# Performance work log

Measured on AMD Instinct MI355X. Metric: run time of the kernel, lower is better.

## Reference

```python
import jax, jax.numpy as jnp
import numpy as np


def setup_inputs() -> dict:
    key = jax.random.key(0)
    kW, kH, kT = jax.random.split(key, 3)
    N, M, rank = 1024, 1024, 64
    W = jax.random.uniform(kW, (N, rank), dtype=jnp.float32)
    H = jax.random.uniform(kH, (rank, M), dtype=jnp.float32)
    tau = jax.random.uniform(kT, (N, rank), dtype=jnp.float32)
    return {"W": W, "H": H, "tau": tau}


def reference(W, H, tau):
    # Vectorized ShiftNMF forward over all M frequency bins at once.
    # Original: for f in range(M): WHt[:, f] = (softplus(W) * exp(-1j*2*pi*f/M * tau)) @ Hf[:, f]
    M = H.shape[1]
    Hf = jnp.fft.fft(jax.nn.softplus(H), axis=1)          # (rank, M) complex64
    Wp = jax.nn.softplus(W)                                # (N, rank)
    freqs = jnp.arange(M, dtype=jnp.float32)               # (M,)
    # phase[n, r, f] = exp(-1j * 2*pi*f/M * tau[n, r])
    phase = jnp.exp((-2j * jnp.pi / M) * tau[:, :, None] * freqs[None, None, :])  # (N, rank, M)
    # WHt[n, f] = sum_r Wp[n, r] * phase[n, r, f] * Hf[r, f]
    WHt = jnp.einsum('nr,nrf,rf->nf', Wp.astype(phase.dtype), phase, Hf)
    return WHt
```

## Files before the change

kernel.cpp:

```cpp
#include <hip/hip_runtime.h>
#include <math.h>

#define M_DIM 1024
#define N_DIM 1024
#define NRANK 64
#define BN 16
#define BF 64

typedef float f32x2 __attribute__((ext_vector_type(2)));

__device__ f32x2 g_Hf[NRANK * M_DIM];

__device__ __forceinline__ float softplus_f(float x) {
    return log1pf(__expf(x));
}

__device__ __forceinline__ float fast_sin_rev(float rev) {
#if __has_builtin(__builtin_amdgcn_sinf)
    return __builtin_amdgcn_sinf(rev);
#else
    return __sinf(rev * 6.28318530717958647f);
#endif
}
__device__ __forceinline__ float fast_cos_rev(float rev) {
#if __has_builtin(__builtin_amdgcn_cosf)
    return __builtin_amdgcn_cosf(rev);
#else
    return __cosf(rev * 6.28318530717958647f);
#endif
}

__global__ __launch_bounds__(512) void fft_rows(const float* __restrict__ H) {
    __shared__ float sre[M_DIM];
    __shared__ float sim[M_DIM];
    const int r = blockIdx.x;
    const int tid = threadIdx.x;

    for (int j = tid; j < M_DIM; j += 512) {
        int src = __brev((unsigned)j) >> 22;
        sre[j] = softplus_f(H[r * M_DIM + src]);
        sim[j] = 0.0f;
    }
    __syncthreads();

    int log2half = 0;
    for (int len = 2; len <= M_DIM; len <<= 1, ++log2half) {
        const int half = len >> 1;
        const int j    = tid & (half - 1);
        const int base = (tid >> log2half) << (log2half + 1);
        const int i0   = base + j;
        const int i1   = i0 + half;
        const float rev = -(float)j / (float)len;
        const float s = fast_sin_rev(rev);
        const float c = fast_cos_rev(rev);
        const float xr = sre[i1], xi = sim[i1];
        const float vr = xr * c - xi * s;
        const float vi = xr * s + xi * c;
        const float ur = sre[i0], ui = sim[i0];
        sre[i0] = ur + vr;  sim[i0] = ui + vi;
        sre[i1] = ur - vr;  sim[i1] = ui - vi;
        __syncthreads();
    }

    for (int j = tid; j < M_DIM; j += 512) {
        g_Hf[r * M_DIM + j] = (f32x2){sre[j], sim[j]};
    }
}

__global__ __launch_bounds__(256) void shiftnmf_main(
    const float* __restrict__ W, const float* __restrict__ tau,
    float* __restrict__ out, int out_elems) {

    __shared__ f32x2  shHf[NRANK][BF];
    __shared__ float4 shC [NRANK][BN + 1];

    const int tid = threadIdx.x;
    const int f0  = blockIdx.x * BF;
    const int n0  = blockIdx.y * BN;

    for (int idx = tid; idx < NRANK * BF; idx += 256) {
        const int rr = idx >> 6, ff = idx & 63;
        shHf[rr][ff] = g_Hf[rr * M_DIM + f0 + ff];
    }
    for (int idx = tid; idx < BN * NRANK; idx += 256) {
        const int nn = idx >> 6, rr = idx & 63;
        const int n  = n0 + nn;
        const float wp = softplus_f(W[n * NRANK + rr]);
        const float a  = (-1.0f / (float)M_DIM) * tau[n * NRANK + rr];
        const float rev16 = a * 16.0f;
        shC[rr][nn] = make_float4(a, wp, fast_cos_rev(rev16), fast_sin_rev(rev16));
    }
    __syncthreads();

    const int fbase = tid & 15;
    const int n_loc = tid >> 4;
    const float fglob = (float)(f0 + fbase);

    f32x2 acc[4] = {{0.f, 0.f}, {0.f, 0.f}, {0.f, 0.f}, {0.f, 0.f}};

    for (int r = 0; r < NRANK; ++r) {
        const float4 cf = shC[r][n_loc];
        const float rev0 = cf.x * fglob;
        f32x2 p;
        p.x = cf.y * fast_cos_rev(rev0);
        p.y = cf.y * fast_sin_rev(rev0);
        const f32x2 st = {cf.z, cf.w};
        #pragma unroll
        for (int k = 0; k < 4; ++k) {
            const f32x2 h = shHf[r][fbase + (k << 4)];
            const f32x2 pneg = {-p.y, p.y};
            acc[k] = __builtin_elementwise_fma(pneg, (f32x2){h.y, h.x}, acc[k]);
            acc[k] = __builtin_elementwise_fma((f32x2){p.x, p.x}, h, acc[k]);
            if (k < 3) {
                const f32x2 t = pneg * (f32x2){st.y, st.x};
                p = __builtin_elementwise_fma((f32x2){p.x, p.x}, st, t);
            }
        }
    }

    #pragma unroll
    for (int k = 0; k < 4; ++k) {
        const int n  = n0 + n_loc;
        const int oi = n * M_DIM + f0 + fbase + (k << 4);
        if (oi < out_elems) out[oi] = acc[k].x;
        const int oj = N_DIM * M_DIM + oi;
        if (oj < out_elems) out[oj] = acc[k].y;
    }
}

extern "C" void kernel_launch(void* const* d_in, const int* in_sizes, int n_in,
                              void* d_out, int out_size, void* d_ws, size_t ws_size,
                              hipStream_t stream) {
    const float* W   = (const float*)d_in[0];
    const float* H   = (const float*)d_in[1];
    const float* tau = (const float*)d_in[2];

    (void)d_ws; (void)ws_size;

    fft_rows<<<NRANK, 512, 0, stream>>>(H);
    shiftnmf_main<<<dim3(M_DIM / BF, N_DIM / BN), 256, 0, stream>>>(
        W, tau, (float*)d_out, out_size);
}
```

Before: 85.12 us.

## Use radix-4 FFT and precompute W/tau coefficients in the FFT kernel

The radix-2 row FFT (10 barrier-separated stages, 512 threads) becomes a radix-4 decimation-in-frequency FFT with 256 threads and far fewer sync stages, writing results with digit-reversed indices. Extra blocks in the same launch precompute the softplus(W), tau phase step and its cos/sin into a global buffer. The main kernel then loads these instead of recomputing them in each of the 16 f-blocks that share an n-tile. This removes redundant transcendental work, but adds a global round trip of float4 coefficients.

```diff
diff --git a/kernel.cpp b/kernel.cpp
--- a/kernel.cpp
+++ b/kernel.cpp
@@ -10,6 +10,7 @@
 typedef float f32x2 __attribute__((ext_vector_type(2)));
 
 __device__ f32x2 g_Hf[NRANK * M_DIM];
+__device__ float4 g_C[N_DIM * NRANK];
 
 __device__ __forceinline__ float softplus_f(float x) {
     return log1pf(__expf(x));
@@ -30,45 +31,94 @@
 #endif
 }
 
-__global__ __launch_bounds__(512) void fft_rows(const float* __restrict__ H) {
-    __shared__ float sre[M_DIM];
-    __shared__ float sim[M_DIM];
-    const int r = blockIdx.x;
-    const int tid = threadIdx.x;
+__device__ __forceinline__ f32x2 cmul(f32x2 a, float c, float s) {
+    return (f32x2){a.x * c - a.y * s, a.x * s + a.y * c};
+}
 
-    for (int j = tid; j < M_DIM; j += 512) {
-        int src = __brev((unsigned)j) >> 22;
-        sre[j] = softplus_f(H[r * M_DIM + src]);
-        sim[j] = 0.0f;
+__global__ __launch_bounds__(256) void fft_rows(
+    const float* __restrict__ H, const float* __restrict__ W,
+    const float* __restrict__ tau) {
+
+    const int b   = blockIdx.x;
+    const int t   = threadIdx.x;
+
+    if (b >= NRANK) {
+        const int base = (b - NRANK) * (256 * 16) + t;
+        #pragma unroll
+        for (int it = 0; it < 16; ++it) {
+            const int idx = base + it * 256;
+            const float wp = softplus_f(W[idx]);
+            const float a  = (-1.0f / (float)M_DIM) * tau[idx];
+            const float rev16 = a * 16.0f;
+            g_C[idx] = make_float4(a, wp, fast_cos_rev(rev16), fast_sin_rev(rev16));
+        }
+        return;
+    }
+
+    __shared__ f32x2 s[M_DIM];
+    const int r = b;
+
+    {
+        const float v0 = softplus_f(H[r * M_DIM + t]);
+        const float v1 = softplus_f(H[r * M_DIM + t + 256]);
+        const float v2 = softplus_f(H[r * M_DIM + t + 512]);
+        const float v3 = softplus_f(H[r * M_DIM + t + 768]);
+        const float u0 = v0 + v2, u1 = v0 - v2;
+        const float u2 = v1 + v3, u3 = v1 - v3;
+        const float j1 = -(float)t * (1.0f / 1024.0f);
+        const float c1 = fast_cos_rev(j1),        s1 = fast_sin_rev(j1);
+        const float c2 = fast_cos_rev(2.0f * j1), s2 = fast_sin_rev(2.0f * j1);
+        const float c3 = fast_cos_rev(3.0f * j1), s3 = fast_sin_rev(3.0f * j1);
+        s[t]       = (f32x2){u0 + u2, 0.0f};
+        s[t + 256] = (f32x2){u1 * c1 + u3 * s1, u1 * s1 - u3 * c1};
+        s[t + 512] = (f32x2){(u0 - u2) * c2,    (u0 - u2) * s2};
+        s[t + 768] = (f32x2){u1 * c3 - u3 * s3, u1 * s3 + u3 * c3};
     }
     __syncthreads();
 
-    int log2half = 0;
-    for (int len = 2; len <= M_DIM; len <<= 1, ++log2half) {
-        const int half = len >> 1;
-        const int j    = tid & (half - 1);
-        const int base = (tid >> log2half) << (log2half + 1);
-        const int i0   = base + j;
-        const int i1   = i0 + half;
-        const float rev = -(float)j / (float)len;
-        const float s = fast_sin_rev(rev);
-        const float c = fast_cos_rev(rev);
-        const float xr = sre[i1], xi = sim[i1];
-        const float vr = xr * c - xi * s;
-        const float vi = xr * s + xi * c;
-        const float ur = sre[i0], ui = sim[i0];
-        sre[i0] = ur + vr;  sim[i0] = ui + vi;
-        sre[i1] = ur - vr;  sim[i1] = ui - vi;
+    #pragma unroll
+    for (int stage = 0; stage < 3; ++stage) {
+        const int log2q = 6 - 2 * stage;
+        const int q     = 1 << log2q;
+        const int j     = t & (q - 1);
+        const int i0    = ((t >> log2q) << (log2q + 2)) + j;
+        const f32x2 a = s[i0], bb = s[i0 + q], c = s[i0 + 2 * q], d = s[i0 + 3 * q];
+        const f32x2 u0 = a + c, u1 = a - c, u2 = bb + d, u3 = bb - d;
+        const float jr = -(float)j / (float)(4 << log2q);
+        const float c1 = fast_cos_rev(jr),        s1 = fast_sin_rev(jr);
+        const float c2 = fast_cos_rev(2.0f * jr), s2 = fast_sin_rev(2.0f * jr);
+        const float c3 = fast_cos_rev(3.0f * jr), s3 = fast_sin_rev(3.0f * jr);
+        const f32x2 m1 = {u1.x + u3.y, u1.y - u3.x};
+        const f32x2 m3 = {u1.x - u3.y, u1.y + u3.x};
+        s[i0]         = u0 + u2;
+        s[i0 + q]     = cmul(m1, c1, s1);
+        s[i0 + 2*q]   = cmul(u0 - u2, c2, s2);
+        s[i0 + 3*q]   = cmul(m3, c3, s3);
         __syncthreads();
     }
 
-    for (int j = tid; j < M_DIM; j += 512) {
-        g_Hf[r * M_DIM + j] = (f32x2){sre[j], sim[j]};
+    {
+        const float4* s4 = reinterpret_cast<const float4*>(s);
+        const float4 p0 = s4[2 * t];
+        const float4 p1 = s4[2 * t + 1];
+        const f32x2 a = {p0.x, p0.y}, bb = {p0.z, p0.w};
+        const f32x2 c = {p1.x, p1.y}, d  = {p1.z, p1.w};
+        const f32x2 u0 = a + c, u1 = a - c, u2 = bb + d, u3 = bb - d;
+        const f32x2 z0 = u0 + u2;
+        const f32x2 z1 = {u1.x + u3.y, u1.y - u3.x};
+        const f32x2 z2 = u0 - u2;
+        const f32x2 z3 = {u1.x - u3.y, u1.y + u3.x};
+        const int dr = ((t & 3) << 6) | (((t >> 2) & 3) << 4) |
+                       (((t >> 4) & 3) << 2) | ((t >> 6) & 3);
+        f32x2* __restrict__ o = g_Hf + r * M_DIM + dr;
+        o[0]   = z0;
+        o[256] = z1;
+        o[512] = z2;
+        o[768] = z3;
     }
 }
 
 __global__ __launch_bounds__(256) void shiftnmf_main(
-    const float* __restrict__ W, const float* __restrict__ tau,
     float* __restrict__ out, int out_elems) {
 
     __shared__ f32x2  shHf[NRANK][BF];
@@ -84,11 +134,7 @@
     }
     for (int idx = tid; idx < BN * NRANK; idx += 256) {
         const int nn = idx >> 6, rr = idx & 63;
-        const int n  = n0 + nn;
-        const float wp = softplus_f(W[n * NRANK + rr]);
-        const float a  = (-1.0f / (float)M_DIM) * tau[n * NRANK + rr];
-        const float rev16 = a * 16.0f;
-        shC[rr][nn] = make_float4(a, wp, fast_cos_rev(rev16), fast_sin_rev(rev16));
+        shC[rr][nn] = g_C[(n0 + nn) * NRANK + rr];
     }
     __syncthreads();
 
@@ -112,8 +158,8 @@
             acc[k] = __builtin_elementwise_fma(pneg, (f32x2){h.y, h.x}, acc[k]);
             acc[k] = __builtin_elementwise_fma((f32x2){p.x, p.x}, h, acc[k]);
             if (k < 3) {
-                const f32x2 t = pneg * (f32x2){st.y, st.x};
-                p = __builtin_elementwise_fma((f32x2){p.x, p.x}, st, t);
+                const f32x2 tswap = pneg * (f32x2){st.y, st.x};
+                p = __builtin_elementwise_fma((f32x2){p.x, p.x}, st, tswap);
             }
         }
     }
@@ -137,7 +183,7 @@
 
     (void)d_ws; (void)ws_size;
 
-    fft_rows<<<NRANK, 512, 0, stream>>>(H);
+    fft_rows<<<NRANK + 16, 256, 0, stream>>>(H, W, tau);
     shiftnmf_main<<<dim3(M_DIM / BF, N_DIM / BN), 256, 0, stream>>>(
-        W, tau, (float*)d_out, out_size);
+        (float*)d_out, out_size);
 }
```

Result: no change. 84.97 us (-0.2%).
